# Kernel tuning notes

Hardware: AMD Instinct MI355X
Metric: run time of the kernel (lower is better)

Reference implementation:

```python
import jax, jax.numpy as jnp
import numpy as np

INPUT_DIMS = (8, 16, 8)
OUTPUT_DIMS = (8, 16, 8)
TT_RANKS = (1, 8, 8, 1)
SUP = 4
OUT_DIM = int(np.prod(OUTPUT_DIMS))


def _glorot(key, shape):
    # GlorotUniform over full core shape (matches keras initializer semantics closely enough
    # for a correctness baseline; exact init values are not part of the math being tested)
    fan_in = shape[0] * shape[1]
    fan_out = shape[2] * shape[3]
    limit = (6.0 / (fan_in + fan_out)) ** 0.5
    return jax.random.uniform(key, shape, jnp.float32, -limit, limit)


def setup_inputs() -> dict:
    key = jax.random.key(0)
    kx, k0, k1, k2 = jax.random.split(key, 4)
    x = jax.random.normal(kx, (2, 2048, 1024), dtype=jnp.float32)
    core0 = _glorot(k0, (TT_RANKS[0], INPUT_DIMS[0], OUTPUT_DIMS[0], TT_RANKS[1], SUP))
    core1 = _glorot(k1, (TT_RANKS[1], INPUT_DIMS[1], OUTPUT_DIMS[1], TT_RANKS[2], SUP))
    core2 = _glorot(k2, (TT_RANKS[2], INPUT_DIMS[2], OUTPUT_DIMS[2], TT_RANKS[3], SUP))
    return {"x": x, "core0": core0, "core1": core1, "core2": core2}


def reference(x, core0, core1, core2):
    B, S, _ = x.shape
    n = B * S
    # [n, i0, i1, i2]
    res = x.reshape(n, *INPUT_DIMS)
    # core0 has leading TT-rank 1 -> squeeze: (i0, o0, r1, s)
    c0 = core0[0]
    # contract input mode 0: n i0 i1 i2 , i0 o0 r1 s -> n o0 i1 i2 r1 s
    res = jnp.einsum('nbcd,bwqs->nwcdqs', res, c0)
    # contract input mode 1 + rank r1: -> n o0 o1 i2 r2 s
    res = jnp.einsum('nwcdqs,qcxrs->nwxdrs', res, core1)
    # contract input mode 2 + rank r2: -> n o0 o1 o2 r3 s  (r3 == 1)
    res = jnp.einsum('nwxdrs,rdyts->nwxyts', res, core2)
    res = jnp.squeeze(res, axis=-2)  # drop trailing rank-1 axis
    out = res.reshape(n, OUT_DIM, SUP)
    return out.reshape(B, S, OUT_DIM, SUP)
```

## Files before the change

kernel.cpp:

```cpp
#include <hip/hip_runtime.h>
#include <stdint.h>

typedef unsigned short u16;
typedef unsigned int u32;
typedef __bf16 bf16x8 __attribute__((ext_vector_type(8)));
typedef float f32x4 __attribute__((ext_vector_type(4)));

#define MFMA16 __builtin_amdgcn_mfma_f32_16x16x32_bf16


__device__ __forceinline__ u16 f2bf(float f) {
    u32 u = __builtin_bit_cast(u32, f);
    u32 r = (u + 0x7FFFu + ((u >> 16) & 1u)) >> 16;
    return (u16)r;
}

__device__ __forceinline__ void gload_lds16(const u16* g, u16* l) {
    __builtin_amdgcn_global_load_lds(
        (const __attribute__((address_space(1))) void*)g,
        (__attribute__((address_space(3))) void*)l,
        16, 0, 0);
}


__global__ __launch_bounds__(256) void pre_kernel(const float* __restrict__ x,
                                                  const float* __restrict__ c0,
                                                  const float* __restrict__ c1,
                                                  const float* __restrict__ c2,
                                                  u16* __restrict__ xb,
                                                  u16* __restrict__ Wt,
                                                  int convBlocks, int nElem) {
    __shared__ float smem[10496];
    const int t = threadIdx.x;

    if ((int)blockIdx.x < convBlocks) {
        int i = (blockIdx.x * 256 + t) * 8;
        if (i + 8 > nElem) return;
        float4 a = *reinterpret_cast<const float4*>(x + i);
        float4 b = *reinterpret_cast<const float4*>(x + i + 4);
        uint4 pk;
        pk.x = (u32)f2bf(a.x) | ((u32)f2bf(a.y) << 16);
        pk.y = (u32)f2bf(a.z) | ((u32)f2bf(a.w) << 16);
        pk.z = (u32)f2bf(b.x) | ((u32)f2bf(b.y) << 16);
        pk.w = (u32)f2bf(b.z) | ((u32)f2bf(b.w) << 16);
        *reinterpret_cast<uint4*>(xb + i) = pk;
        return;
    }

    float* l_c0 = smem;
    float* l_c1 = smem + 256;
    float* l_c2 = smem + 4352;
    float* l_w1 = smem + 6400;

    const int bid = blockIdx.x - convBlocks;
    const int bc = bid >> 2;
    const int part = bid & 3;
    const int b = bc >> 4, c = bc & 15;

    l_c0[t] = c0[b * 256 + t];
#pragma unroll
    for (int q = 0; q < 8; ++q) {
        l_c1[q * 512 + t]       = c1[(q * 16 + c) * 512 + t];
        l_c1[q * 512 + t + 256] = c1[(q * 16 + c) * 512 + t + 256];
    }
#pragma unroll
    for (int j = 0; j < 8; ++j) l_c2[t + 256 * j] = c2[t + 256 * j];
    __syncthreads();

#pragma unroll
    for (int j = 0; j < 4; ++j) {
        int idx = t + 256 * (part * 4 + j);
        int s = idx & 3;
        int r = (idx >> 2) & 7;
        int xx = (idx >> 5) & 15;
        int w = idx >> 9;
        float acc = 0.f;
#pragma unroll
        for (int q = 0; q < 8; ++q)
            acc += l_c0[(w * 8 + q) * 4 + s] * l_c1[q * 512 + (xx * 8 + r) * 4 + s];
        l_w1[idx] = acc;
    }
    __syncthreads();

#pragma unroll
    for (int j = 0; j < 4; ++j) {
        int idx = t + 256 * (part * 4 + j);
        int s = idx & 3;
        int y = (idx >> 2) & 7;
        int xx = (idx >> 5) & 15;
        int w = idx >> 9;
        float acc[8] = {0.f, 0.f, 0.f, 0.f, 0.f, 0.f, 0.f, 0.f};
#pragma unroll
        for (int r = 0; r < 8; ++r) {
            float w1 = l_w1[((w * 16 + xx) * 8 + r) * 4 + s];
#pragma unroll
            for (int d = 0; d < 8; ++d)
                acc[d] += w1 * l_c2[((r * 8 + d) * 8 + y) * 4 + s];
        }
        uint4 pk;
        pk.x = (u32)f2bf(acc[0]) | ((u32)f2bf(acc[1]) << 16);
        pk.y = (u32)f2bf(acc[2]) | ((u32)f2bf(acc[3]) << 16);
        pk.z = (u32)f2bf(acc[4]) | ((u32)f2bf(acc[5]) << 16);
        pk.w = (u32)f2bf(acc[6]) | ((u32)f2bf(acc[7]) << 16);
        *reinterpret_cast<uint4*>(&Wt[(size_t)idx * 1024 + b * 128 + c * 8]) = pk;
    }
}


#define SLOT_U16 16384
#define HALF_U16 8192

#define BAR() __builtin_amdgcn_s_barrier()
#define LGKM0() do { asm volatile("s_waitcnt lgkmcnt(0)" ::: "memory"); \
                     __builtin_amdgcn_sched_barrier(0); } while (0)
#define VMW0() do { asm volatile("s_waitcnt vmcnt(0)" ::: "memory"); \
                    __builtin_amdgcn_sched_barrier(0); } while (0)

__global__ __launch_bounds__(512, 2) void gemm256_kernel(const u16* __restrict__ A,
                                                         const u16* __restrict__ B,
                                                         float* __restrict__ C,
                                                         int M, int N, int K) {
    __shared__ u16 As[2 * SLOT_U16];
    __shared__ u16 Bs[2 * SLOT_U16];

    const int t   = threadIdx.x;
    const int ln  = t & 63;
    const int wid = t >> 6;
    const int wr  = wid >> 2;
    const int wc  = wid & 3;
    const int m0  = blockIdx.y * 256;
    const int n0  = blockIdx.x * 256;
    const int NT  = K >> 6;

    const int frow  = ln & 15;
    const int arow  = wr * 128 + frow;
    const int brow  = wc * 64 + frow;
    const int koff0 = (((ln >> 4) ^ (ln & 7)) * 8);
    const int koff1 = koff0 ^ 32;

    const int ca = t, cb = t + 512;
    const int pra = ca >> 3, lsa = (ca & 7) ^ ((ca >> 3) & 7);
    const int prb = cb >> 3, lsb = (cb & 7) ^ ((cb >> 3) & 7);

    f32x4 acc[8][4] = {};

    auto stage_half = [&](const u16* g ,
                          u16* l ) {
        gload_lds16(g + (size_t)pra * K + lsa * 8, l + ca * 8);
        gload_lds16(g + (size_t)prb * K + lsb * 8, l + cb * 8);
    };

    stage_half(B + (size_t)n0 * K,          Bs);
    stage_half(B + (size_t)(n0 + 128) * K,  Bs + HALF_U16);
    stage_half(A + (size_t)m0 * K,          As);
    stage_half(A + (size_t)(m0 + 128) * K,  As + HALF_U16);
    VMW0();
    BAR();

    for (int kt = 0; kt < NT; ++kt) {
        const u16* Ab = As + (kt & 1) * SLOT_U16;
        const u16* Bb = Bs + (kt & 1) * SLOT_U16;
        u16* An = As + ((kt + 1) & 1) * SLOT_U16;
        u16* Bn = Bs + ((kt + 1) & 1) * SLOT_U16;
        const bool pf = (kt + 1) < NT;
        const int kc = (kt + 1) * 64;

        bf16x8 bf[4][2];
        bf16x8 a0k0, a0k1, a1k0, a1k1;

#define LOAD_A_PAIR(R0, R1)                                                  \
        {   const u16* ap0 = Ab + (size_t)(arow + (R0)) * 64;                \
            const u16* ap1 = Ab + (size_t)(arow + (R1)) * 64;                \
            a0k0 = *reinterpret_cast<const bf16x8*>(ap0 + koff0);            \
            a0k1 = *reinterpret_cast<const bf16x8*>(ap0 + koff1);            \
            a1k0 = *reinterpret_cast<const bf16x8*>(ap1 + koff0);            \
            a1k1 = *reinterpret_cast<const bf16x8*>(ap1 + koff1);  }

#define MFMA_PAIR(F0, F1)                                                    \
        _Pragma("unroll")                                                    \
        for (int n = 0; n < 4; ++n) {                                        \
            acc[F0][n] = MFMA16(a0k0, bf[n][0], acc[F0][n], 0, 0, 0);        \
            acc[F0][n] = MFMA16(a0k1, bf[n][1], acc[F0][n], 0, 0, 0);        \
            acc[F1][n] = MFMA16(a1k0, bf[n][0], acc[F1][n], 0, 0, 0);        \
            acc[F1][n] = MFMA16(a1k1, bf[n][1], acc[F1][n], 0, 0, 0);        \
        }

#pragma unroll
        for (int n = 0; n < 4; ++n) {
            const u16* bp = Bb + (size_t)(brow + n * 16) * 64;
            bf[n][0] = *reinterpret_cast<const bf16x8*>(bp + koff0);
            bf[n][1] = *reinterpret_cast<const bf16x8*>(bp + koff1);
        }
        LOAD_A_PAIR(0, 16);
        if (pf) {
            stage_half(B + (size_t)n0 * K + kc,         Bn);
            stage_half(B + (size_t)(n0 + 128) * K + kc, Bn + HALF_U16);
        }
        BAR();
        LGKM0();
        __builtin_amdgcn_s_setprio(1);
        MFMA_PAIR(0, 1);
        __builtin_amdgcn_s_setprio(0);
        BAR();

        LOAD_A_PAIR(32, 48);
        if (pf) {
            stage_half(A + (size_t)m0 * K + kc,         An);
            stage_half(A + (size_t)(m0 + 128) * K + kc, An + HALF_U16);
        }
        BAR();
        LGKM0();
        __builtin_amdgcn_s_setprio(1);
        MFMA_PAIR(2, 3);
        __builtin_amdgcn_s_setprio(0);
        BAR();

        LOAD_A_PAIR(64, 80);
        BAR();
        LGKM0();
        __builtin_amdgcn_s_setprio(1);
        MFMA_PAIR(4, 5);
        __builtin_amdgcn_s_setprio(0);
        BAR();

        LOAD_A_PAIR(96, 112);
        BAR();
        LGKM0();
        __builtin_amdgcn_s_setprio(1);
        MFMA_PAIR(6, 7);
        __builtin_amdgcn_s_setprio(0);
        if (pf) VMW0();
        BAR();

#undef LOAD_A_PAIR
#undef MFMA_PAIR
    }

    const int cr = (ln >> 4) * 4;
    const int cc = ln & 15;
#pragma unroll
    for (int fm = 0; fm < 8; ++fm) {
#pragma unroll
        for (int r = 0; r < 4; ++r) {
            int row = m0 + wr * 128 + fm * 16 + cr + r;
            float* p = C + (size_t)row * N + n0 + wc * 64 + cc;
#pragma unroll
            for (int fn = 0; fn < 4; ++fn)
                p[fn * 16] = acc[fm][fn][r];
        }
    }
}


extern "C" void kernel_launch(void* const* d_in, const int* in_sizes, int n_in,
                              void* d_out, int out_size, void* d_ws, size_t ws_size,
                              hipStream_t stream) {
    const float* x  = (const float*)d_in[0];
    const float* c0 = (const float*)d_in[1];
    const float* c1 = (const float*)d_in[2];
    const float* c2 = (const float*)d_in[3];
    float* out = (float*)d_out;

    const int K = 1024;
    const int N = 4096;
    const int M = in_sizes[0] / K;

    u16* xb = (u16*)d_ws;
    u16* Wt = (u16*)d_ws + (size_t)M * K;

    const int convBlocks = (M * K) / (256 * 8);
    pre_kernel<<<convBlocks + 512, 256, 0, stream>>>(x, c0, c1, c2, xb, Wt,
                                                     convBlocks, M * K);

    dim3 g(N / 256, M / 256);
    gemm256_kernel<<<g, 512, 0, stream>>>(xb, Wt, out, M, N, K);
}
```

Before: 58.40 us.

## Remap GEMM blocks per XCD, fix LDS swizzle keys, drop manual waitcnts

Launches the GEMM on a 1D grid and remaps each block ID so that blocks on the same XCD cover a compact 2x(8x4) tile region, aiming for better L2 reuse of A and B. The LDS read swizzle now uses each fragment's actual row (arow/brow) instead of the lane index, so reads match the row-based XOR pattern used when staging. The explicit s_waitcnt and sched_barrier macros are removed, and the compiler is left to insert waits, with __syncthreads at the prologue and loop end. This may loosen the hand-tuned schedule, and it relies on the compiler placing the vmcnt wait before the barrier for correctness.

```diff
diff --git a/kernel.cpp b/kernel.cpp
--- a/kernel.cpp
+++ b/kernel.cpp
@@ -111,10 +111,6 @@
 #define HALF_U16 8192
 
 #define BAR() __builtin_amdgcn_s_barrier()
-#define LGKM0() do { asm volatile("s_waitcnt lgkmcnt(0)" ::: "memory"); \
-                     __builtin_amdgcn_sched_barrier(0); } while (0)
-#define VMW0() do { asm volatile("s_waitcnt vmcnt(0)" ::: "memory"); \
-                    __builtin_amdgcn_sched_barrier(0); } while (0)
 
 __global__ __launch_bounds__(512, 2) void gemm256_kernel(const u16* __restrict__ A,
                                                          const u16* __restrict__ B,
@@ -128,15 +124,24 @@
     const int wid = t >> 6;
     const int wr  = wid >> 2;
     const int wc  = wid & 3;
-    const int m0  = blockIdx.y * 256;
-    const int n0  = blockIdx.x * 256;
+
+    const int bid = blockIdx.x;
+    const int xcd = bid & 7;
+    const int r   = bid >> 3;
+    const int bx  = (xcd & 1) * 8 + (r & 7);
+    const int by  = (xcd >> 1) * 4 + (r >> 3);
+    const int m0  = by * 256;
+    const int n0  = bx * 256;
     const int NT  = K >> 6;
 
     const int frow  = ln & 15;
+    const int ks    = ln >> 4;
     const int arow  = wr * 128 + frow;
     const int brow  = wc * 64 + frow;
-    const int koff0 = (((ln >> 4) ^ (ln & 7)) * 8);
-    const int koff1 = koff0 ^ 32;
+    const int koffa0 = ((ks ^ (arow & 7)) * 8);
+    const int koffa1 = koffa0 ^ 32;
+    const int koffb0 = ((ks ^ (brow & 7)) * 8);
+    const int koffb1 = koffb0 ^ 32;
 
     const int ca = t, cb = t + 512;
     const int pra = ca >> 3, lsa = (ca & 7) ^ ((ca >> 3) & 7);
@@ -154,8 +159,7 @@
     stage_half(B + (size_t)(n0 + 128) * K,  Bs + HALF_U16);
     stage_half(A + (size_t)m0 * K,          As);
     stage_half(A + (size_t)(m0 + 128) * K,  As + HALF_U16);
-    VMW0();
-    BAR();
+    __syncthreads();
 
     for (int kt = 0; kt < NT; ++kt) {
         const u16* Ab = As + (kt & 1) * SLOT_U16;
@@ -171,10 +175,10 @@
 #define LOAD_A_PAIR(R0, R1)                                                  \
         {   const u16* ap0 = Ab + (size_t)(arow + (R0)) * 64;                \
             const u16* ap1 = Ab + (size_t)(arow + (R1)) * 64;                \
-            a0k0 = *reinterpret_cast<const bf16x8*>(ap0 + koff0);            \
-            a0k1 = *reinterpret_cast<const bf16x8*>(ap0 + koff1);            \
-            a1k0 = *reinterpret_cast<const bf16x8*>(ap1 + koff0);            \
-            a1k1 = *reinterpret_cast<const bf16x8*>(ap1 + koff1);  }
+            a0k0 = *reinterpret_cast<const bf16x8*>(ap0 + koffa0);           \
+            a0k1 = *reinterpret_cast<const bf16x8*>(ap0 + koffa1);           \
+            a1k0 = *reinterpret_cast<const bf16x8*>(ap1 + koffa0);           \
+            a1k1 = *reinterpret_cast<const bf16x8*>(ap1 + koffa1);  }
 
 #define MFMA_PAIR(F0, F1)                                                    \
         _Pragma("unroll")                                                    \
@@ -188,8 +192,8 @@
 #pragma unroll
         for (int n = 0; n < 4; ++n) {
             const u16* bp = Bb + (size_t)(brow + n * 16) * 64;
-            bf[n][0] = *reinterpret_cast<const bf16x8*>(bp + koff0);
-            bf[n][1] = *reinterpret_cast<const bf16x8*>(bp + koff1);
+            bf[n][0] = *reinterpret_cast<const bf16x8*>(bp + koffb0);
+            bf[n][1] = *reinterpret_cast<const bf16x8*>(bp + koffb1);
         }
         LOAD_A_PAIR(0, 16);
         if (pf) {
@@ -197,7 +201,6 @@
             stage_half(B + (size_t)(n0 + 128) * K + kc, Bn + HALF_U16);
         }
         BAR();
-        LGKM0();
         __builtin_amdgcn_s_setprio(1);
         MFMA_PAIR(0, 1);
         __builtin_amdgcn_s_setprio(0);
@@ -209,7 +212,6 @@
             stage_half(A + (size_t)(m0 + 128) * K + kc, An + HALF_U16);
         }
         BAR();
-        LGKM0();
         __builtin_amdgcn_s_setprio(1);
         MFMA_PAIR(2, 3);
         __builtin_amdgcn_s_setprio(0);
@@ -217,7 +219,6 @@
 
         LOAD_A_PAIR(64, 80);
         BAR();
-        LGKM0();
         __builtin_amdgcn_s_setprio(1);
         MFMA_PAIR(4, 5);
         __builtin_amdgcn_s_setprio(0);
@@ -225,12 +226,10 @@
 
         LOAD_A_PAIR(96, 112);
         BAR();
-        LGKM0();
         __builtin_amdgcn_s_setprio(1);
         MFMA_PAIR(6, 7);
         __builtin_amdgcn_s_setprio(0);
-        if (pf) VMW0();
-        BAR();
+        __syncthreads();
 
 #undef LOAD_A_PAIR
 #undef MFMA_PAIR
@@ -241,12 +240,12 @@
 #pragma unroll
     for (int fm = 0; fm < 8; ++fm) {
 #pragma unroll
-        for (int r = 0; r < 4; ++r) {
-            int row = m0 + wr * 128 + fm * 16 + cr + r;
+        for (int rr = 0; rr < 4; ++rr) {
+            int row = m0 + wr * 128 + fm * 16 + cr + rr;
             float* p = C + (size_t)row * N + n0 + wc * 64 + cc;
 #pragma unroll
             for (int fn = 0; fn < 4; ++fn)
-                p[fn * 16] = acc[fm][fn][r];
+                p[fn * 16] = acc[fm][fn][rr];
         }
     }
 }
@@ -272,6 +271,5 @@
     pre_kernel<<<convBlocks + 512, 256, 0, stream>>>(x, c0, c1, c2, xb, Wt,
                                                      convBlocks, M * K);
 
-    dim3 g(N / 256, M / 256);
-    gemm256_kernel<<<g, 512, 0, stream>>>(xb, Wt, out, M, N, K);
-}
+    gemm256_kernel<<<(N / 256) * (M / 256), 512, 0, stream>>>(xb, Wt, out, M, N, K);
+}
```

After: 57.32 us. About the same (-1.8%).
